# Kernel tuning notes

Hardware: AMD Instinct MI355X
Metric: run time of the kernel (lower is better)

## Reference

```python
import jax, jax.numpy as jnp
import numpy as np

N_SITES = 1024
A_PER_SITE = 2
R_PER_ALLELE = 16
N_ALLELES = N_SITES * A_PER_SITE
N_READS = N_ALLELES * R_PER_ALLELE
C_IN, C, L = 16, 32, 150


def conv1d(x, w, stride=1, dilation=1, pad=2):
    return jax.lax.conv_general_dilated(
        x, w, (stride,), [(pad, pad)], rhs_dilation=(dilation,),
        dimension_numbers=('NCH', 'OIH', 'NCH'))


def reduce_slots(d, slots):
    # cumsum-diff segmented sum over dim 0, exactly as torch reduceSlots
    res = jnp.cumsum(d, axis=0)
    idx = jnp.cumsum(slots) - 1
    sel = res[idx]
    padded = jnp.concatenate([jnp.zeros_like(sel[:1]), sel[:-1]], axis=0)
    return sel - padded


def xattn(allele, site0, site1, wq, wk, wv, wo):
    # cross-attention: allele features query the two expanded site-feature streams
    q = jnp.einsum('oc,ncl->nol', wq, allele)
    kv = jnp.concatenate([site0, site1], axis=-1)  # [Na, C, 2*L']
    k = jnp.einsum('oc,ncl->nol', wk, kv)
    v = jnp.einsum('oc,ncl->nol', wv, kv)
    scores = jnp.einsum('ncl,ncm->nlm', q, k) / np.float32(np.sqrt(C))
    ctx = jnp.einsum('nlm,ncm->ncl', jax.nn.softmax(scores, axis=-1), v)
    return jnp.mean(allele + ctx, axis=-1) @ wo.T  # [Na, 2]


def setup_inputs():
    ks = jax.random.split(jax.random.key(0), 24)
    w = lambda i, shape: jax.random.normal(ks[i], shape, jnp.float32) * 0.05
    return {
        'tensors0': jax.random.normal(ks[0], (N_READS, C_IN, L), jnp.float32),
        'tensors1': jax.random.normal(ks[1], (N_READS, C_IN, L), jnp.float32),
        'conv0_w': w(2, (C, C_IN, 5)), 'conv1_w': w(3, (C, C_IN, 5)),
        'comp0_w': w(4, (C, C, 3)), 'comp1_w': w(5, (C, C, 3)), 'comp2_w': w(6, (C, C, 3)),
        'xq0': w(7, (C, C)), 'xk0': w(8, (C, C)), 'xv0': w(9, (C, C)), 'xo0': w(10, (2, C)),
        'xq1': w(11, (C, C)), 'xk1': w(12, (C, C)), 'xv1': w(13, (C, C)), 'xo1': w(14, (2, C)),
        'xq2': w(15, (C, C)), 'xk2': w(16, (C, C)), 'xv2': w(17, (C, C)), 'xo2': w(18, (2, C)),
        'comb_w': w(19, (C, 2 * C)), 'meta_w': w(20, (3, 2 * C)), 'meta_b': w(21, (3,)),
        'num_alleles_per_site': jnp.full((N_SITES,), A_PER_SITE, jnp.int32),
        'num_reads0': jnp.full((N_ALLELES,), R_PER_ALLELE, jnp.int32),
        'num_reads1': jnp.full((N_ALLELES,), R_PER_ALLELE, jnp.int32),
    }


def reference(tensors0, tensors1, conv0_w, conv1_w, comp0_w, comp1_w, comp2_w,
              xq0, xk0, xv0, xo0, xq1, xk1, xv1, xo1, xq2, xk2, xv2, xo2,
              comb_w, meta_w, meta_b, num_alleles_per_site, num_reads0, num_reads1):
    compressor = lambda x, w: jax.nn.relu(conv1d(x, w, stride=2, dilation=2, pad=2))

    def compress_and_predict(red_allele, comp_w, xw):
        cfa = compressor(red_allele, comp_w)                       # [Na, C, L']
        rfs = reduce_slots(red_allele, num_alleles_per_site)       # [Ns, C, L]
        cfs0 = compressor(rfs, comp_w)                             # [Ns, C, L']
        exp0 = jnp.repeat(cfs0, num_alleles_per_site, axis=0, total_repeat_length=N_ALLELES)
        cfs1 = reduce_slots(cfa, num_alleles_per_site)             # [Ns, C, L']
        exp1 = jnp.repeat(cfs1, num_alleles_per_site, axis=0, total_repeat_length=N_ALLELES)
        return xattn(cfa, exp0, exp1, *xw), (cfs0, cfs1)

    rc0 = jax.nn.relu(conv1d(tensors0, conv0_w, pad=2))            # [Nr, C, L]
    red0 = reduce_slots(rc0, num_reads0)                           # [Na, C, L]
    e0, _ = compress_and_predict(red0, comp0_w, (xq0, xk0, xv0, xo0))

    rc1 = jax.nn.relu(conv1d(tensors1, conv1_w, pad=2))
    red1 = reduce_slots(rc1, num_reads1)
    e1, _ = compress_and_predict(red1, comp1_w, (xq1, xk1, xv1, xo1))

    red2 = jax.nn.relu(jnp.einsum('oc,ncl->nol', comb_w, jnp.concatenate([red0, red1], axis=1)))
    e2, (s0, s1) = compress_and_predict(red2, comp2_w, (xq2, xk2, xv2, xo2))

    meta_feat = jnp.mean(jnp.concatenate([s0, s1], axis=1), axis=-1)  # [Ns, 2C]
    meta = jax.nn.softmax(meta_feat @ meta_w.T + meta_b, axis=-1)     # [Ns, 3]
    return (jnp.stack([e0, e1, e2]), meta)
```

## Files before the change

kernel.cpp:

```cpp
#include <hip/hip_runtime.h>
#include <math.h>

#define NS 1024
#define NA 2048
#define CIN 16
#define CC 32
#define LL 150
#define LC 75

typedef __attribute__((ext_vector_type(8))) short short8;
typedef __attribute__((ext_vector_type(4))) float float4v;

__device__ __forceinline__ unsigned short f2bf(float f) {
  unsigned int u = __float_as_uint(f);
  unsigned int r = (u + 0x7FFFu + ((u >> 16) & 1u)) >> 16;
  return (unsigned short)r;
}

__device__ __forceinline__ unsigned int pkbf(float lo, float hi) {
  return (unsigned int)f2bf(lo) | ((unsigned int)f2bf(hi) << 16);
}

__device__ __forceinline__ float bflo(unsigned int u) { return __uint_as_float(u << 16); }
__device__ __forceinline__ float bfhi(unsigned int u) { return __uint_as_float(u & 0xffff0000u); }

#if __has_builtin(__builtin_amdgcn_fdot2_f32_bf16)
typedef __attribute__((ext_vector_type(2))) __bf16 bf16x2;
__device__ __forceinline__ float bdot2(unsigned int a, unsigned int b, float c) {
  return __builtin_amdgcn_fdot2_f32_bf16(__builtin_bit_cast(bf16x2, a),
                                         __builtin_bit_cast(bf16x2, b), c, false);
}
#else
__device__ __forceinline__ float bdot2(unsigned int a, unsigned int b, float c) {
  return c + bflo(a) * bflo(b) + bfhi(a) * bfhi(b);
}
#endif

__global__ __launch_bounds__(256) void k_conv_sum_mfma(const float* __restrict__ x,
                                                       const float* __restrict__ w,
                                                       float* __restrict__ red) {
  __shared__ unsigned short xs[2][154 * 32];
  const int a = blockIdx.x;
  const int tid = threadIdx.x;
  const int lane = tid & 63;
  const int wv = tid >> 6;

  short8 afr[2][3];
  {
    const int mrow = lane & 15;
    const int h = lane >> 4;
    for (int mt = 0; mt < 2; ++mt) {
      const int c = mt * 16 + mrow;
      for (int s = 0; s < 3; ++s) {
        short8 f;
#pragma unroll
        for (int j = 0; j < 8; ++j) {
          int ic = 4 * h + (j >> 1);
          int tap = 2 * s + (j & 1);
          float wval = (tap < 5) ? w[c * 80 + ic * 5 + tap] : 0.f;
          f[j] = (short)f2bf(wval);
        }
        afr[mt][s] = f;
      }
    }
  }

  float4v sum[2][3];
#pragma unroll
  for (int mt = 0; mt < 2; ++mt)
#pragma unroll
    for (int nt = 0; nt < 3; ++nt) sum[mt][nt] = (float4v)(0.f);

  const int nbase = wv * 48;
  const int nrow = lane & 15;
  const int hh = lane >> 4;
  const float4v zf = (float4v)(0.f);

  auto stage = [&](int r, int buf) {
    const float* xr = x + (size_t)(a * 16 + r) * (CIN * LL);
    unsigned int* xb32 = (unsigned int*)xs[buf];
    for (int idx = tid; idx < 16 * 38; idx += 256) {
      const int ic = idx & 15;
      const int seg = idx >> 4;
      const int l0 = seg * 4;
      const float* row = xr + ic * LL;
      float v0, v1, v2, v3, v4;
      if (seg < 37) {
        float2 u = *(const float2*)(row + l0);
        float2 u2 = *(const float2*)(row + l0 + 2);
        v0 = u.x; v1 = u.y; v2 = u2.x; v3 = u2.y;
        v4 = row[l0 + 4];
      } else {
        float2 u = *(const float2*)(row + 148);
        v0 = u.x; v1 = u.y; v2 = 0.f; v3 = 0.f; v4 = 0.f;
      }
      const int hb = 4 * (ic >> 2) + (ic & 3);
      unsigned int* b32 = xb32 + 16 * (l0 + 2) + hb;
      b32[0]  = pkbf(v0, v1);
      b32[16] = pkbf(v1, v2);
      b32[32] = pkbf(v2, v3);
      b32[48] = pkbf(v3, v4);
    }
    if (tid < 32) {
      const int ic = tid & 15;
      const int which = tid >> 4;
      const int hb = 4 * (ic >> 2) + (ic & 3);
      xb32[16 * which + hb] = which ? pkbf(0.f, xr[ic * LL]) : 0u;
    }
  };

  stage(0, 0);
  __syncthreads();

  for (int r = 0; r < 16; ++r) {
    const int cur = r & 1;
    if (r + 1 < 16) stage(r + 1, cur ^ 1);

    float4v acc[2][3];
#pragma unroll
    for (int s = 0; s < 3; ++s) {
#pragma unroll
      for (int nt = 0; nt < 3; ++nt) {
        int p = nbase + nt * 16 + nrow + 2 * s;
        if (p >= 154) p -= 154;
        short8 bfrag = *(const short8*)&xs[cur][(4 * p + hh) * 8];
#pragma unroll
        for (int mt = 0; mt < 2; ++mt) {
          acc[mt][nt] = __builtin_amdgcn_mfma_f32_16x16x32_bf16(
              afr[mt][s], bfrag, (s == 0) ? zf : acc[mt][nt], 0, 0, 0);
        }
      }
    }
#pragma unroll
    for (int mt = 0; mt < 2; ++mt)
#pragma unroll
      for (int nt = 0; nt < 3; ++nt)
#pragma unroll
        for (int q = 0; q < 4; ++q) sum[mt][nt][q] += fmaxf(acc[mt][nt][q], 0.f);

    __syncthreads();
  }

  const int ccol = lane & 15;
  const int crow4 = (lane >> 4) * 4;
  for (int mt = 0; mt < 2; ++mt)
    for (int nt = 0; nt < 3; ++nt) {
      int l = nbase + nt * 16 + ccol;
      if (l < LL) {
#pragma unroll
        for (int q = 0; q < 4; ++q) {
          int c = mt * 16 + crow4 + q;
          red[(size_t)a * (CC * LL) + c * LL + l] = sum[mt][nt][q];
        }
      }
    }
}

__global__ __launch_bounds__(256) void k_comb(const float* __restrict__ red0,
                                              const float* __restrict__ red1,
                                              const float* __restrict__ cw,
                                              float* __restrict__ out) {
  __shared__ float ins[64][152];
  __shared__ float cwl[64][CC];
  const int a = blockIdx.x;
  const int tid = threadIdx.x;

  for (int i = tid; i < 64 * CC; i += 256) {
    int c = i & 31; int c2 = i >> 5;
    cwl[c2][c] = cw[c * 64 + c2];
  }
  for (int i = tid; i < CC * LL; i += 256) {
    int c2 = i / LL; int l = i - c2 * LL;
    ins[c2][l] = red0[(size_t)a * (CC * LL) + i];
    ins[32 + c2][l] = red1[(size_t)a * (CC * LL) + i];
  }
  __syncthreads();

  const int c = tid & 31;
  const int lg = tid >> 5;
  const int l0 = lg * 19;
  const int nl = (LL - l0 < 19) ? (LL - l0) : 19;
  float v[19];
#pragma unroll
  for (int j = 0; j < 19; ++j) v[j] = 0.f;
  for (int c2 = 0; c2 < 64; ++c2) {
    float wv = cwl[c2][c];
#pragma unroll
    for (int j = 0; j < 19; ++j) v[j] += wv * ins[c2][l0 + j];
  }
  float* o = out + (size_t)a * (CC * LL) + c * LL + l0;
  for (int j = 0; j < nl; ++j) o[j] = fmaxf(v[j], 0.f);
}

#define BWK   2400
#define BWV   3456
#define BWQ   4512
#define BQT   5568
#define BCF   7968
#define KB_US 15936
#define VB_US 20864
#define BPART 3456
#define BMS   3968
#define ARENA 13056
#define FIN0  0
#define FIN1  4992
#define FWS   9984

__device__ __forceinline__ void attn_phase_d(float* __restrict__ ar, int g, int t,
                                             float& ms) {
  unsigned short* aru = (unsigned short*)ar;
  const float scale = 0.17677669529663687f;
  const int rb_us = g * 760;
#pragma unroll 1
  for (int cc = 0; cc < 2; ++cc) {
    const int ch = g + 8 * cc;
    if (ch >= 15) break;
    const int r0 = ch * 5;

    float2 acc[5][3];
#pragma unroll
    for (int i = 0; i < 5; ++i)
#pragma unroll
      for (int u = 0; u < 3; ++u) acc[i][u] = make_float2(0.f, 0.f);

#pragma unroll 1
    for (int c2 = 0; c2 < 32; c2 += 2) {
      float2 q01[5];
#pragma unroll
      for (int i = 0; i < 5; ++i) q01[i] = *(const float2*)&ar[BQT + (r0 + i) * 32 + c2];
      const int k0 = KB_US + c2 * 154 + 2 * t;
      const int k1 = k0 + 154;
      unsigned int a0 = *(const unsigned int*)&aru[k0];
      unsigned int a1 = *(const unsigned int*)&aru[k0 + 64];
      unsigned int a2 = *(const unsigned int*)&aru[k0 + 128];
      unsigned int b0 = *(const unsigned int*)&aru[k1];
      unsigned int b1 = *(const unsigned int*)&aru[k1 + 64];
      unsigned int b2 = *(const unsigned int*)&aru[k1 + 128];
      float ka0x = bflo(a0), ka0y = bfhi(a0);
      float ka1x = bflo(a1), ka1y = bfhi(a1);
      float ka2x = bflo(a2), ka2y = bfhi(a2);
      float kb0x = bflo(b0), kb0y = bfhi(b0);
      float kb1x = bflo(b1), kb1y = bfhi(b1);
      float kb2x = bflo(b2), kb2y = bfhi(b2);
#pragma unroll
      for (int i = 0; i < 5; ++i) {
        acc[i][0].x += q01[i].x * ka0x + q01[i].y * kb0x;
        acc[i][0].y += q01[i].x * ka0y + q01[i].y * kb0y;
        acc[i][1].x += q01[i].x * ka1x + q01[i].y * kb1x;
        acc[i][1].y += q01[i].x * ka1y + q01[i].y * kb1y;
        acc[i][2].x += q01[i].x * ka2x + q01[i].y * kb2x;
        acc[i][2].y += q01[i].x * ka2y + q01[i].y * kb2y;
      }
    }

    float inv[5];
#pragma unroll
    for (int i = 0; i < 5; ++i) {
      float s0x = acc[i][0].x * scale, s0y = acc[i][0].y * scale;
      float s1x = acc[i][1].x * scale, s1y = acc[i][1].y * scale;
      float s2x = acc[i][2].x * scale, s2y = acc[i][2].y * scale;
      if (t >= 11) { s2x = -1e30f; s2y = -1e30f; }
      float mx = fmaxf(fmaxf(fmaxf(s0x, s0y), fmaxf(s1x, s1y)), fmaxf(s2x, s2y));
#pragma unroll
      for (int off = 16; off > 0; off >>= 1) mx = fmaxf(mx, __shfl_xor(mx, off, 32));
      float p0x = __expf(s0x - mx), p0y = __expf(s0y - mx);
      float p1x = __expf(s1x - mx), p1y = __expf(s1y - mx);
      float p2x = __expf(s2x - mx), p2y = __expf(s2y - mx);
      float ss = p0x + p0y + p1x + p1y + p2x + p2y;
#pragma unroll
      for (int off = 16; off > 0; off >>= 1) ss += __shfl_xor(ss, off, 32);
      inv[i] = 1.f / ss;
      const int rw = rb_us + i * 152 + 2 * t;
      *(unsigned int*)&aru[rw]      = pkbf(p0x, p0y);
      *(unsigned int*)&aru[rw + 64] = pkbf(p1x, p1y);
      if (t <= 11) *(unsigned int*)&aru[rw + 128] = pkbf(p2x, p2y);
    }

    float pv[5] = {0.f, 0.f, 0.f, 0.f, 0.f};
    const int vb = VB_US + t * 164;
    for (int mq = 0; mq < 38; ++mq) {
      uint2 vv = *(const uint2*)&aru[vb + 4 * mq];
#pragma unroll
      for (int i = 0; i < 5; ++i) {
        uint2 pp = *(const uint2*)&aru[rb_us + i * 152 + 4 * mq];
        pv[i] = bdot2(pp.x, vv.x, pv[i]);
        pv[i] = bdot2(pp.y, vv.y, pv[i]);
      }
    }
#pragma unroll
    for (int i = 0; i < 5; ++i) ms += pv[i] * inv[i];
  }
}

__global__ __launch_bounds__(256) void k_cattn(const float* __restrict__ red,
                                               const float* __restrict__ cw,
                                               const float* __restrict__ wq,
                                               const float* __restrict__ wk,
                                               const float* __restrict__ wv,
                                               const float* __restrict__ wo,
                                               float* __restrict__ cfa,
                                               float* __restrict__ cfs,
                                               float* __restrict__ eout,
                                               int wg) {
  __shared__ float ar[ARENA];
  unsigned short* aru = (unsigned short*)ar;
  const int s = blockIdx.x;
  const int tid = threadIdx.x;
  const int g = tid >> 5;
  const int t = tid & 31;

  float* a0g = cfa + (size_t)(2 * s) * (CC * LC);
  float* a1g = a0g + CC * LC;
  float* sgw = cfs + (size_t)s * (CC * LC);

  for (int i = tid; i < CC * 3 * CC; i += 256) {
    int c = i & 31; int kk = i >> 5;
    ar[FWS + kk * 32 + c] = cw[c * (CC * 3) + kk];
  }
  if (tid < CC) {
    ar[FIN0 + tid * 156 + 0] = 0.f; ar[FIN0 + tid * 156 + 1] = 0.f;
    ar[FIN0 + tid * 156 + 152] = 0.f; ar[FIN0 + tid * 156 + 153] = 0.f;
    ar[FIN1 + tid * 156 + 0] = 0.f; ar[FIN1 + tid * 156 + 1] = 0.f;
    ar[FIN1 + tid * 156 + 152] = 0.f; ar[FIN1 + tid * 156 + 153] = 0.f;
  }
  {
    const float* s0 = red + (size_t)(2 * s) * (CC * LL);
    const float* s1 = s0 + CC * LL;
    for (int i = tid; i < CC * LL; i += 256) {
      int ic = i / LL; int l = i - ic * LL;
      ar[FIN0 + ic * 156 + l + 2] = s0[i];
      ar[FIN1 + ic * 156 + l + 2] = s1[i];
    }
  }
  __syncthreads();

  const int j0 = g * 10;
  const int nj = (LC - j0 < 10) ? (LC - j0) : 10;
  float v0[10], v1[10];
#pragma unroll
  for (int j = 0; j < 10; ++j) { v0[j] = 0.f; v1[j] = 0.f; }
  for (int ic = 0; ic < CC; ++ic) {
    float w0 = ar[FWS + (ic * 3 + 0) * 32 + t];
    float w1 = ar[FWS + (ic * 3 + 1) * 32 + t];
    float w2 = ar[FWS + (ic * 3 + 2) * 32 + t];
    float xa[12], xb[12];
#pragma unroll
    for (int i = 0; i < 12; ++i) {
      xa[i] = ar[FIN0 + ic * 156 + 2 * j0 + 2 * i];
      xb[i] = ar[FIN1 + ic * 156 + 2 * j0 + 2 * i];
    }
#pragma unroll
    for (int j = 0; j < 10; ++j) {
      v0[j] += w0 * xa[j] + w1 * xa[j + 1] + w2 * xa[j + 2];
      v1[j] += w0 * xb[j] + w1 * xb[j + 1] + w2 * xb[j + 2];
    }
  }
  __syncthreads();

  for (int j = 0; j < nj; ++j) {
    const int jj = j0 + j;
    float r0 = fmaxf(v0[j], 0.f);
    float r1 = fmaxf(v1[j], 0.f);
    float cs = fmaxf(v0[j] + v1[j], 0.f);
    aru[jj * 32 + t]        = f2bf(cs);
    aru[(75 + jj) * 32 + t] = f2bf(r0 + r1);
    ar[BCF + t * 77 + jj]   = r0;
    a1g[t * 75 + jj] = r1;
    if (wg) {
      a0g[t * 75 + jj] = r0;
      sgw[t * 75 + jj] = cs;
    }
  }
  for (int i = tid; i < CC * CC; i += 256) {
    int o = i >> 5, ii = i & 31;
    ar[BWQ + ii * 33 + o] = wq[i];
    ar[BWK + ii * 33 + o] = wk[i];
    ar[BWV + ii * 33 + o] = wv[i];
  }
  __syncthreads();

  float cfp0 = 0.f;
  {
    float wqc[32];
#pragma unroll
    for (int ii = 0; ii < 32; ++ii) wqc[ii] = ar[BWQ + ii * 33 + t];
    for (int row = g; row < 75; row += 8) {
      float acc = 0.f;
#pragma unroll
      for (int ii = 0; ii < 32; ++ii) acc += wqc[ii] * ar[BCF + ii * 77 + row];
      ar[BQT + row * 32 + t] = acc;
      cfp0 += ar[BCF + t * 77 + row];
    }
  }
  __syncthreads();

  {
    unsigned int wk2[16], wv2[16];
    {
      float wkc[32], wvc[32];
#pragma unroll
      for (int ii = 0; ii < 32; ++ii) {
        wkc[ii] = ar[BWK + ii * 33 + t];
        wvc[ii] = ar[BWV + ii * 33 + t];
      }
#pragma unroll
      for (int j = 0; j < 16; ++j) {
        wk2[j] = pkbf(wkc[2 * j], wkc[2 * j + 1]);
        wv2[j] = pkbf(wvc[2 * j], wvc[2 * j + 1]);
      }
    }
    for (int idx = tid; idx < CC * LL; idx += 256) {
      int o = idx & 31, m = idx >> 5;
      const unsigned int* kvrow = (const unsigned int*)&aru[m * 32];
      float ka = 0.f, va = 0.f;
#pragma unroll
      for (int j = 0; j < 16; ++j) {
        unsigned int u = kvrow[j];
        ka = bdot2(wk2[j], u, ka);
        va = bdot2(wv2[j], u, va);
      }
      aru[KB_US + o * 154 + m] = f2bf(ka);
      aru[VB_US + o * 164 + m] = f2bf(va);
    }
    if (tid < 32) *(unsigned int*)&aru[VB_US + tid * 164 + 150] = 0u;
  }
  __syncthreads();

  float ms0 = 0.f;
  attn_phase_d(ar, g, t, ms0);
  __syncthreads();

  float cfp1 = 0.f;
  {
    float wqc[32];
#pragma unroll
    for (int ii = 0; ii < 32; ++ii) wqc[ii] = ar[BWQ + ii * 33 + t];
    for (int row = g; row < 75; row += 8) {
      float acc = 0.f;
#pragma unroll
      for (int ii = 0; ii < 32; ++ii) acc += wqc[ii] * a1g[ii * 75 + row];
      ar[BQT + row * 32 + t] = acc;
      cfp1 += a1g[t * 75 + row];
    }
  }
  __syncthreads();

  float ms1 = 0.f;
  attn_phase_d(ar, g, t, ms1);

  ar[BPART + g * 32 + t]       = cfp0 + ms0;
  ar[BPART + 256 + g * 32 + t] = cfp1 + ms1;
  __syncthreads();

  if (tid < 64) {
    int al = tid >> 5, tt = tid & 31;
    float tot = 0.f;
#pragma unroll
    for (int gg = 0; gg < 8; ++gg) tot += ar[BPART + al * 256 + gg * 32 + tt];
    ar[BMS + al * 32 + tt] = tot * (1.f / 75.f);
  }
  __syncthreads();
  if (tid < 4) {
    int al = tid >> 1, o2 = tid & 1;
    float e = 0.f;
#pragma unroll
    for (int c2 = 0; c2 < CC; ++c2) e += wo[o2 * CC + c2] * ar[BMS + al * 32 + c2];
    eout[s * 4 + tid] = e;
  }
}

__global__ __launch_bounds__(64) void k_meta(const float* __restrict__ cfs0,
                                             const float* __restrict__ cfa2,
                                             const float* __restrict__ mw,
                                             const float* __restrict__ mb,
                                             float* __restrict__ mout) {
  __shared__ float feat[64];
  __shared__ float lgt[3];
  const int s = blockIdx.x;
  const int tid = threadIdx.x;
  float f = 0.f;
  if (tid < 32) {
    const float* p = cfs0 + (size_t)s * (CC * LC) + tid * LC;
    for (int l = 0; l < LC; ++l) f += p[l];
  } else {
    const float* p0 = cfa2 + (size_t)(2 * s) * (CC * LC) + (tid - 32) * LC;
    const float* p1 = cfa2 + (size_t)(2 * s + 1) * (CC * LC) + (tid - 32) * LC;
    for (int l = 0; l < LC; ++l) f += p0[l] + p1[l];
  }
  feat[tid] = f * (1.f / 75.f);
  __syncthreads();
  if (tid < 3) {
    float acc2 = mb[tid];
    for (int c2 = 0; c2 < 64; ++c2) acc2 += mw[tid * 64 + c2] * feat[c2];
    lgt[tid] = acc2;
  }
  __syncthreads();
  if (tid < 3) {
    float mx = fmaxf(lgt[0], fmaxf(lgt[1], lgt[2]));
    float e0 = __expf(lgt[0] - mx), e1 = __expf(lgt[1] - mx), e2 = __expf(lgt[2] - mx);
    mout[s * 3 + tid] = __expf(lgt[tid] - mx) / (e0 + e1 + e2);
  }
}

extern "C" void kernel_launch(void* const* d_in, const int* in_sizes, int n_in,
                              void* d_out, int out_size, void* d_ws, size_t ws_size,
                              hipStream_t stream) {
  const float* t0      = (const float*)d_in[0];
  const float* t1      = (const float*)d_in[1];
  const float* conv0_w = (const float*)d_in[2];
  const float* conv1_w = (const float*)d_in[3];
  const float* comp0_w = (const float*)d_in[4];
  const float* comp1_w = (const float*)d_in[5];
  const float* comp2_w = (const float*)d_in[6];
  const float* xq0 = (const float*)d_in[7];
  const float* xk0 = (const float*)d_in[8];
  const float* xv0 = (const float*)d_in[9];
  const float* xo0 = (const float*)d_in[10];
  const float* xq1 = (const float*)d_in[11];
  const float* xk1 = (const float*)d_in[12];
  const float* xv1 = (const float*)d_in[13];
  const float* xo1 = (const float*)d_in[14];
  const float* xq2 = (const float*)d_in[15];
  const float* xk2 = (const float*)d_in[16];
  const float* xv2 = (const float*)d_in[17];
  const float* xo2 = (const float*)d_in[18];
  const float* comb_w = (const float*)d_in[19];
  const float* meta_w = (const float*)d_in[20];
  const float* meta_b = (const float*)d_in[21];

  float* wsf  = (float*)d_ws;
  float* red0 = wsf;
  float* red1 = red0 + (size_t)NA * CC * LL;
  float* cfa  = red1 + (size_t)NA * CC * LL;
  float* cfs0 = cfa + (size_t)NA * CC * LC;
  float* out  = (float*)d_out;

  k_conv_sum_mfma<<<NA, 256, 0, stream>>>(t0, conv0_w, red0);
  k_conv_sum_mfma<<<NA, 256, 0, stream>>>(t1, conv1_w, red1);

  k_cattn<<<NS, 256, 0, stream>>>(red0, comp0_w, xq0, xk0, xv0, xo0,
                                  cfa, cfs0, out + 0, 0);
  k_cattn<<<NS, 256, 0, stream>>>(red1, comp1_w, xq1, xk1, xv1, xo1,
                                  cfa, cfs0, out + 2 * NA, 0);

  k_comb<<<NA, 256, 0, stream>>>(red0, red1, comb_w, red0);
  k_cattn<<<NS, 256, 0, stream>>>(red0, comp2_w, xq2, xk2, xv2, xo2,
                                  cfa, cfs0, out + 4 * NA, 1);

  k_meta<<<NS, 64, 0, stream>>>(cfs0, cfa, meta_w, meta_b, out + 6 * NA);
}
```

Measured before the change: 1.231 ms.

## Store compressed allele features and Q in bf16 LDS, keep cf1 out of global

The compressed per-allele features for both alleles are now kept in LDS as bf16 rows, so the second allele's Q projection no longer rereads them from global memory. The allele-1 global store is only issued when the writeback flag is set. Q is computed with packed bf16 dot products from register-resident packed weights and stored as bf16, and the LDS arena is relaid out to fit these buffers. This lowers LDS footprint and global traffic, but Q and the mean features lose precision, and a barrier is added after the second attention phase.

After: 1.204 ms. 2.2% less time.

```diff
diff --git a/kernel.cpp b/kernel.cpp
--- a/kernel.cpp
+++ b/kernel.cpp
@@ -192,25 +192,27 @@
   for (int j = 0; j < nl; ++j) o[j] = fmaxf(v[j], 0.f);
 }
 
-#define BWK   2400
-#define BWV   3456
-#define BWQ   4512
-#define BQT   5568
-#define BCF   7968
-#define KB_US 15936
-#define VB_US 20864
-#define BPART 3456
-#define BMS   3968
-#define ARENA 13056
-#define FIN0  0
-#define FIN1  4992
-#define FWS   9984
+#define AKV_US 0
+#define BWK    2400
+#define BWV    3456
+#define BWQ    4512
+#define QT_US  4800
+#define BPART  3600
+#define BMS    4112
+#define CF0_US 11136
+#define CF1_US 13536
+#define KB_US  15936
+#define VB_US  20864
+#define ARENA  13056
+#define FIN0   0
+#define FIN1   4928
+#define FWS    9856
 
 __device__ __forceinline__ void attn_phase_d(float* __restrict__ ar, int g, int t,
                                              float& ms) {
   unsigned short* aru = (unsigned short*)ar;
   const float scale = 0.17677669529663687f;
-  const int rb_us = g * 760;
+  const int rb_us = (g < 6) ? g * 760 : 9024 + (g - 6) * 760;
 #pragma unroll 1
   for (int cc = 0; cc < 2; ++cc) {
     const int ch = g + 8 * cc;
@@ -227,7 +229,10 @@
     for (int c2 = 0; c2 < 32; c2 += 2) {
       float2 q01[5];
 #pragma unroll
-      for (int i = 0; i < 5; ++i) q01[i] = *(const float2*)&ar[BQT + (r0 + i) * 32 + c2];
+      for (int i = 0; i < 5; ++i) {
+        unsigned int qp = *(const unsigned int*)&aru[QT_US + (r0 + i) * 32 + c2];
+        q01[i] = make_float2(bflo(qp), bfhi(qp));
+      }
       const int k0 = KB_US + c2 * 154 + 2 * t;
       const int k1 = k0 + 154;
       unsigned int a0 = *(const unsigned int*)&aru[k0];
@@ -318,18 +323,18 @@
     ar[FWS + kk * 32 + c] = cw[c * (CC * 3) + kk];
   }
   if (tid < CC) {
-    ar[FIN0 + tid * 156 + 0] = 0.f; ar[FIN0 + tid * 156 + 1] = 0.f;
-    ar[FIN0 + tid * 156 + 152] = 0.f; ar[FIN0 + tid * 156 + 153] = 0.f;
-    ar[FIN1 + tid * 156 + 0] = 0.f; ar[FIN1 + tid * 156 + 1] = 0.f;
-    ar[FIN1 + tid * 156 + 152] = 0.f; ar[FIN1 + tid * 156 + 153] = 0.f;
+    ar[FIN0 + tid * 154 + 0] = 0.f; ar[FIN0 + tid * 154 + 1] = 0.f;
+    ar[FIN0 + tid * 154 + 152] = 0.f; ar[FIN0 + tid * 154 + 153] = 0.f;
+    ar[FIN1 + tid * 154 + 0] = 0.f; ar[FIN1 + tid * 154 + 1] = 0.f;
+    ar[FIN1 + tid * 154 + 152] = 0.f; ar[FIN1 + tid * 154 + 153] = 0.f;
   }
   {
     const float* s0 = red + (size_t)(2 * s) * (CC * LL);
     const float* s1 = s0 + CC * LL;
     for (int i = tid; i < CC * LL; i += 256) {
       int ic = i / LL; int l = i - ic * LL;
-      ar[FIN0 + ic * 156 + l + 2] = s0[i];
-      ar[FIN1 + ic * 156 + l + 2] = s1[i];
+      ar[FIN0 + ic * 154 + l + 2] = s0[i];
+      ar[FIN1 + ic * 154 + l + 2] = s1[i];
     }
   }
   __syncthreads();
@@ -346,8 +351,8 @@
     float xa[12], xb[12];
 #pragma unroll
     for (int i = 0; i < 12; ++i) {
-      xa[i] = ar[FIN0 + ic * 156 + 2 * j0 + 2 * i];
-      xb[i] = ar[FIN1 + ic * 156 + 2 * j0 + 2 * i];
+      xa[i] = ar[FIN0 + ic * 154 + 2 * j0 + 2 * i];
+      xb[i] = ar[FIN1 + ic * 154 + 2 * j0 + 2 * i];
     }
 #pragma unroll
     for (int j = 0; j < 10; ++j) {
@@ -362,12 +367,13 @@
     float r0 = fmaxf(v0[j], 0.f);
     float r1 = fmaxf(v1[j], 0.f);
     float cs = fmaxf(v0[j] + v1[j], 0.f);
-    aru[jj * 32 + t]        = f2bf(cs);
-    aru[(75 + jj) * 32 + t] = f2bf(r0 + r1);
-    ar[BCF + t * 77 + jj]   = r0;
-    a1g[t * 75 + jj] = r1;
+    aru[AKV_US + jj * 32 + t]        = f2bf(cs);
+    aru[AKV_US + (75 + jj) * 32 + t] = f2bf(r0 + r1);
+    aru[CF0_US + jj * 32 + t]        = f2bf(r0);
+    aru[CF1_US + jj * 32 + t]        = f2bf(r1);
     if (wg) {
       a0g[t * 75 + jj] = r0;
+      a1g[t * 75 + jj] = r1;
       sgw[t * 75 + jj] = cs;
     }
   }
@@ -379,39 +385,39 @@
   }
   __syncthreads();
 
+  unsigned int wq2[16], wk2[16], wv2[16];
+  {
+    float wqc[32], wkc[32], wvc[32];
+#pragma unroll
+    for (int ii = 0; ii < 32; ++ii) {
+      wqc[ii] = ar[BWQ + ii * 33 + t];
+      wkc[ii] = ar[BWK + ii * 33 + t];
+      wvc[ii] = ar[BWV + ii * 33 + t];
+    }
+#pragma unroll
+    for (int j = 0; j < 16; ++j) {
+      wq2[j] = pkbf(wqc[2 * j], wqc[2 * j + 1]);
+      wk2[j] = pkbf(wkc[2 * j], wkc[2 * j + 1]);
+      wv2[j] = pkbf(wvc[2 * j], wvc[2 * j + 1]);
+    }
+  }
+  __syncthreads();
+
   float cfp0 = 0.f;
+  for (int row = g; row < 75; row += 8) {
+    const unsigned int* cr = (const unsigned int*)&aru[CF0_US + row * 32];
+    float acc = 0.f;
+#pragma unroll
+    for (int j = 0; j < 16; ++j) acc = bdot2(wq2[j], cr[j], acc);
+    aru[QT_US + row * 32 + t] = f2bf(acc);
+    cfp0 += bflo((unsigned int)aru[CF0_US + row * 32 + t]);
+  }
+  __syncthreads();
+
   {
-    float wqc[32];
-#pragma unroll
-    for (int ii = 0; ii < 32; ++ii) wqc[ii] = ar[BWQ + ii * 33 + t];
-    for (int row = g; row < 75; row += 8) {
-      float acc = 0.f;
-#pragma unroll
-      for (int ii = 0; ii < 32; ++ii) acc += wqc[ii] * ar[BCF + ii * 77 + row];
-      ar[BQT + row * 32 + t] = acc;
-      cfp0 += ar[BCF + t * 77 + row];
-    }
-  }
-  __syncthreads();
-
-  {
-    unsigned int wk2[16], wv2[16];
-    {
-      float wkc[32], wvc[32];
-#pragma unroll
-      for (int ii = 0; ii < 32; ++ii) {
-        wkc[ii] = ar[BWK + ii * 33 + t];
-        wvc[ii] = ar[BWV + ii * 33 + t];
-      }
-#pragma unroll
-      for (int j = 0; j < 16; ++j) {
-        wk2[j] = pkbf(wkc[2 * j], wkc[2 * j + 1]);
-        wv2[j] = pkbf(wvc[2 * j], wvc[2 * j + 1]);
-      }
-    }
     for (int idx = tid; idx < CC * LL; idx += 256) {
       int o = idx & 31, m = idx >> 5;
-      const unsigned int* kvrow = (const unsigned int*)&aru[m * 32];
+      const unsigned int* kvrow = (const unsigned int*)&aru[AKV_US + m * 32];
       float ka = 0.f, va = 0.f;
 #pragma unroll
       for (int j = 0; j < 16; ++j) {
@@ -431,22 +437,19 @@
   __syncthreads();
 
   float cfp1 = 0.f;
-  {
-    float wqc[32];
-#pragma unroll
-    for (int ii = 0; ii < 32; ++ii) wqc[ii] = ar[BWQ + ii * 33 + t];
-    for (int row = g; row < 75; row += 8) {
-      float acc = 0.f;
-#pragma unroll
-      for (int ii = 0; ii < 32; ++ii) acc += wqc[ii] * a1g[ii * 75 + row];
-      ar[BQT + row * 32 + t] = acc;
-      cfp1 += a1g[t * 75 + row];
-    }
+  for (int row = g; row < 75; row += 8) {
+    const unsigned int* cr = (const unsigned int*)&aru[CF1_US + row * 32];
+    float acc = 0.f;
+#pragma unroll
+    for (int j = 0; j < 16; ++j) acc = bdot2(wq2[j], cr[j], acc);
+    aru[QT_US + row * 32 + t] = f2bf(acc);
+    cfp1 += bflo((unsigned int)aru[CF1_US + row * 32 + t]);
   }
   __syncthreads();
 
   float ms1 = 0.f;
   attn_phase_d(ar, g, t, ms1);
+  __syncthreads();
 
   ar[BPART + g * 32 + t]       = cfp0 + ms0;
   ar[BPART + 256 + g * 32 + t] = cfp1 + ms1;
```
